# Kernel tuning notes

Hardware: AMD Instinct MI355X
Metric: run time of the kernel (lower is better)

The kernel has to match this reference:

```python
import jax, jax.numpy as jnp
import numpy as np
import math

B, T, N, D = 8, 12, 500, 512  # batch, time(heads), nodes, K*d
FACTOR = 5
SAMPLE_K = min(FACTOR * math.ceil(math.log(N)), N)  # = 35, also n_top (N_Q == N_K)
W_SCALE = 0.02


def setup_inputs() -> dict:
    key = jax.random.key(0)
    ks = jax.random.split(key, 9)
    f32 = jnp.float32
    return {
        "X":   jax.random.normal(ks[0], (B, T, N, D), f32),
        "STE": jax.random.normal(ks[1], (B, T, N, D), f32),
        "Wq":  jax.random.normal(ks[2], (2 * D, D), f32) * W_SCALE,
        "bq":  jnp.zeros((D,), f32),
        "Wk":  jax.random.normal(ks[3], (2 * D, D), f32) * W_SCALE,
        "bk":  jnp.zeros((D,), f32),
        "Wv":  jax.random.normal(ks[4], (2 * D, D), f32) * W_SCALE,
        "bv":  jnp.zeros((D,), f32),
        "sample_idx": jax.random.randint(ks[5], (N, SAMPLE_K), 0, N, jnp.int32),
    }


def reference(X, STE, Wq, bq, Wk, bk, Wv, bv, sample_idx):
    # concat spatial features with spatio-temporal embedding -> projections
    Xc = jnp.concatenate([X, STE], axis=-1)                  # [B,T,N,2D]
    q = jax.nn.relu(Xc @ Wq + bq)                            # [B,T,N,D]
    k = jax.nn.relu(Xc @ Wk + bk)
    v = jax.nn.relu(Xc @ Wv + bv)

    n_top = SAMPLE_K
    # _prob_QK: sampled Q-K scores. Since SAMPLE_K*D >> N, computing the full
    # [B,T,N,N] score matrix and gathering the sampled columns is strictly
    # cheaper in memory than materializing K_sample [B,T,N,S,D] as torch does;
    # the math (Q_K_sample values) is identical.
    scores_full = jnp.einsum('bhld,bhmd->bhlm', q, k)        # [B,T,N,N]
    QK_sample = jnp.take_along_axis(
        scores_full, sample_idx[None, None, :, :], axis=3)   # [B,T,N,S]
    # sparsity measure M = max - mean (mean over L_K = N)
    M = QK_sample.max(axis=-1) - QK_sample.sum(axis=-1) / N  # [B,T,N]
    _, idx = jax.lax.top_k(M, n_top)                         # [B,T,n_top]

    # reduced-query full attention scores (gather rows of full scores == Q_reduce @ K^T)
    scores = jnp.take_along_axis(scores_full, idx[..., None], axis=2)  # [B,T,u,N]
    scores = scores * (1.0 / math.sqrt(D))

    # ProbMask (mask_flag=True): causal mask per selected query position
    j = jnp.arange(N)
    mask = j[None, None, None, :] > idx[..., None]           # [B,T,u,N]
    scores = jnp.where(mask, -jnp.inf, scores)
    attn = jax.nn.softmax(scores, axis=-1)                   # [B,T,u,N]
    ctx_new = jnp.einsum('bhun,bhnd->bhud', attn, v)         # [B,T,u,D]

    # initial context = causal cumsum of V, then scatter-update selected queries
    context = jnp.cumsum(v, axis=2)                          # [B,T,N,D]
    bi = jnp.arange(B)[:, None, None]
    hi = jnp.arange(T)[None, :, None]
    context = context.at[bi, hi, idx].set(ctx_new)
    # .transpose(2,1) in torch -> swap axes 1 and 2
    return context.transpose(0, 2, 1, 3)                     # [B,N,T,D]
```

## Files before the change

### kernel.cpp

```cpp
#include <hip/hip_runtime.h>
#include <math.h>

#define B_    8
#define T_    12
#define BT    96
#define NN    500
#define DD    512
#define KK    1024
#define SK    35
#define MROWS 48000

typedef __bf16 bf16x8 __attribute__((ext_vector_type(8)));
typedef float f32x4 __attribute__((ext_vector_type(4)));
typedef unsigned short u16;
typedef unsigned int u32;
typedef u16 ushort8_t __attribute__((ext_vector_type(8)));
typedef u16 ushort4_t __attribute__((ext_vector_type(4)));

__device__ __forceinline__ u16 bf_hi(float x) {
  __bf16 h = (__bf16)x;
  return __builtin_bit_cast(u16, h);
}
__device__ __forceinline__ float bf_tof(u16 b) {
  unsigned int u = ((unsigned int)b) << 16;
  return __builtin_bit_cast(float, u);
}

__device__ __forceinline__ int lds_off(int row, int kq) {
  return row * 32 + ((kq ^ ((row >> 1) & 3)) * 8);
}

__device__ __forceinline__ void gload_lds16(const u16* g, u16* l) {
  __builtin_amdgcn_global_load_lds(
      (const __attribute__((address_space(1))) u32*)g,
      (__attribute__((address_space(3))) u32*)l, 16, 0, 0);
}

__global__ __launch_bounds__(256) void convW_kernel(
    const float* __restrict__ W, u16* __restrict__ Bth, u16* __restrict__ Btl)
{
  const int n = blockIdx.x;
  const int k0 = threadIdx.x * 4;
  float xs[4];
#pragma unroll
  for (int j = 0; j < 4; ++j) xs[j] = W[(size_t)(k0 + j) * 512 + n];
  ushort4_t hi, lo;
#pragma unroll
  for (int j = 0; j < 4; ++j) {
    u16 h = bf_hi(xs[j]);
    hi[j] = h;
    lo[j] = bf_hi(xs[j] - bf_tof(h));
  }
  *(ushort4_t*)(Bth + (size_t)n * 1024 + k0) = hi;
  *(ushort4_t*)(Btl + (size_t)n * 1024 + k0) = lo;
}

template<int PASSES>
__global__ __launch_bounds__(256) void mfma_proj(
    const float* __restrict__ X, const float* __restrict__ STE,
    const u16* __restrict__ Bth, const u16* __restrict__ Btl,
    const float* __restrict__ bias, float* __restrict__ out)
{
  constexpr int NT = (PASSES == 3) ? 4 : 2;
  __shared__ u16 ldsbuf[2 * NT * 4096];
  const int tid = threadIdx.x;
  const int lane = tid & 63;
  const int wid = tid >> 6;
  const int wm = wid >> 1, wn = wid & 1;
  const int orig = blockIdx.x;
  const int xcd = orig & 7, pos = orig >> 3;
  const int wg = (xcd < 4 ? xcd * 188 : 752 + (xcd - 4) * 187) + pos;
  const int r0 = (wg >> 2) * 128;
  const int c0 = (wg & 3) * 128;
  const int fr = lane & 15, fk = lane >> 4;
  const int rin = lane >> 2;
  const int qq  = lane & 3;

  f32x4 acc[4][4];
#pragma unroll
  for (int m = 0; m < 4; ++m)
#pragma unroll
    for (int n = 0; n < 4; ++n) acc[m][n] = f32x4{0.f, 0.f, 0.f, 0.f};

  auto STAGE = [&](int buf, int kt) {
    u16* bAh = ldsbuf + buf * NT * 4096;
    u16* bBh = bAh + 4096;
    u16* bAl = bAh + 8192;
    u16* bBl = bAh + 12288;
    const int kk0 = kt * 32;
    float4 a0[2], a1[2];
#pragma unroll
    for (int p = 0; p < 2; ++p) {
      const int c = tid + p * 256;
      const int row = c >> 2, kc = c & 3;
      const int col = kk0 + kc * 8;
      const float* src = (col < 512)
          ? (X + (size_t)(r0 + row) * 512 + col)
          : (STE + (size_t)(r0 + row) * 512 + (col - 512));
      a0[p] = *(const float4*)src;
      a1[p] = *(const float4*)(src + 4);
    }
#pragma unroll
    for (int i = 0; i < 2; ++i) {
      const int ch = wid * 2 + i;
      const int row = ch * 16 + rin;
      const int kq = qq ^ ((row >> 1) & 3);
      const size_t gb = (size_t)(c0 + row) * 1024 + kk0 + kq * 8;
      gload_lds16(Bth + gb, bBh + ch * 512);
      if (PASSES == 3) gload_lds16(Btl + gb, bBl + ch * 512);
    }
#pragma unroll
    for (int p = 0; p < 2; ++p) {
      const int c = tid + p * 256;
      const int row = c >> 2, kc = c & 3;
      const int dst = lds_off(row, kc);
      float xs[8] = {a0[p].x, a0[p].y, a0[p].z, a0[p].w,
                     a1[p].x, a1[p].y, a1[p].z, a1[p].w};
      ushort8_t hi, lo;
#pragma unroll
      for (int j = 0; j < 8; ++j) {
        u16 h = bf_hi(xs[j]);
        hi[j] = h;
        if (PASSES == 3) lo[j] = bf_hi(xs[j] - bf_tof(h));
      }
      *(ushort8_t*)&bAh[dst] = hi;
      if (PASSES == 3) *(ushort8_t*)&bAl[dst] = lo;
    }
  };

  STAGE(0, 0);
  __syncthreads();
  int cur = 0;
  for (int kt = 0; kt < 32; ++kt) {
    if (kt + 1 < 32) STAGE(cur ^ 1, kt + 1);
    u16* bAh = ldsbuf + cur * NT * 4096;
    u16* bBh = bAh + 4096;
    u16* bAl = bAh + 8192;
    u16* bBl = bAh + 12288;
    bf16x8 ah[4], al[4];
#pragma unroll
    for (int m = 0; m < 4; ++m) {
      const int off = lds_off(wm * 64 + m * 16 + fr, fk);
      ah[m] = *(const bf16x8*)&bAh[off];
      if (PASSES == 3) al[m] = *(const bf16x8*)&bAl[off];
    }
#pragma unroll
    for (int n = 0; n < 4; ++n) {
      const int off = lds_off(wn * 64 + n * 16 + fr, fk);
      bf16x8 bh = *(const bf16x8*)&bBh[off];
      bf16x8 bl;
      if (PASSES == 3) bl = *(const bf16x8*)&bBl[off];
#pragma unroll
      for (int m = 0; m < 4; ++m) {
        acc[m][n] = __builtin_amdgcn_mfma_f32_16x16x32_bf16(
            ah[m], bh, acc[m][n], 0, 0, 0);
        if (PASSES == 3) {
          acc[m][n] = __builtin_amdgcn_mfma_f32_16x16x32_bf16(
              ah[m], bl, acc[m][n], 0, 0, 0);
          acc[m][n] = __builtin_amdgcn_mfma_f32_16x16x32_bf16(
              al[m], bh, acc[m][n], 0, 0, 0);
        }
      }
    }
    __syncthreads();
    cur ^= 1;
  }

#pragma unroll
  for (int n = 0; n < 4; ++n) {
    const int col = c0 + wn * 64 + n * 16 + fr;
    const float bb = bias[col];
#pragma unroll
    for (int m = 0; m < 4; ++m) {
      const int rowb = r0 + wm * 64 + m * 16 + fk * 4;
#pragma unroll
      for (int r = 0; r < 4; ++r)
        out[(size_t)(rowb + r) * 512 + col] = fmaxf(acc[m][n][r] + bb, 0.f);
    }
  }
}

__global__ __launch_bounds__(256) void sampled_M_kernel(
    const float* __restrict__ q, const float* __restrict__ k,
    const int* __restrict__ sidx, float* __restrict__ Mout)
{
  const int tid = threadIdx.x;
  const int lane = tid & 63, wid = tid >> 6;
  const int bid = blockIdx.x;
  const int xcd = bid & 7, j = bid >> 3;
  const int btg = j / 125, ub = j - btg * 125;
  const int bt = btg * 8 + xcd;
  const int nn = ub * 4 + wid;
  const int n = bt * NN + nn;
  const float* qrow = q + (size_t)n * DD + lane * 8;
  float4 q0 = *(const float4*)qrow;
  float4 q1 = *(const float4*)(qrow + 4);
  const float* kbase = k + (size_t)bt * NN * DD;
  float mx = -INFINITY, sm = 0.f;
  for (int s = 0; s < SK; ++s) {
    int m = sidx[nn * SK + s];
    const float* krow = kbase + (size_t)m * DD + lane * 8;
    float4 k0 = *(const float4*)krow;
    float4 k1 = *(const float4*)(krow + 4);
    float ss = q0.x*k0.x + q0.y*k0.y + q0.z*k0.z + q0.w*k0.w
             + q1.x*k1.x + q1.y*k1.y + q1.z*k1.z + q1.w*k1.w;
#pragma unroll
    for (int off = 32; off > 0; off >>= 1) ss += __shfl_xor(ss, off);
    mx = fmaxf(mx, ss);
    sm += ss;
  }
  if (lane == 0) Mout[n] = mx - sm * (1.0f / (float)NN);
}

__global__ __launch_bounds__(256) void topk_kernel(
    const float* __restrict__ Mb, int* __restrict__ idxb,
    int* __restrict__ sqi, int* __restrict__ su)
{
  const int bt = blockIdx.x;
  const int tid = threadIdx.x;
  __shared__ float mv[NN];
  __shared__ float rv[256];
  __shared__ int ri[256];
  __shared__ int qsel[SK];
  for (int n = tid; n < NN; n += 256) mv[n] = Mb[(size_t)bt * NN + n];
  __syncthreads();
  for (int it = 0; it < SK; ++it) {
    float bv = -INFINITY; int bi = NN;
    for (int n = tid; n < NN; n += 256) {
      float x = mv[n];
      if (x > bv) { bv = x; bi = n; }
    }
    rv[tid] = bv; ri[tid] = bi;
    __syncthreads();
    for (int sft = 128; sft > 0; sft >>= 1) {
      if (tid < sft) {
        float xv = rv[tid + sft]; int xi = ri[tid + sft];
        if (xv > rv[tid] || (xv == rv[tid] && xi < ri[tid])) {
          rv[tid] = xv; ri[tid] = xi;
        }
      }
      __syncthreads();
    }
    if (tid == 0) {
      idxb[bt * SK + it] = ri[0];
      qsel[it] = ri[0];
      mv[ri[0]] = -INFINITY;
    }
    __syncthreads();
  }
  if (tid < SK) {
    int myqi = qsel[tid];
    int rank = 0;
    for (int j = 0; j < SK; ++j) rank += (qsel[j] < myqi);
    sqi[bt * SK + rank] = myqi;
    su[bt * SK + rank] = tid;
  }
}

__global__ __launch_bounds__(256) void attn_part_kernel(
    const float* __restrict__ q, const float* __restrict__ k,
    const float* __restrict__ v, const int* __restrict__ sqi,
    float* __restrict__ pO, float* __restrict__ pm, float* __restrict__ pl)
{
  const int bid = blockIdx.x;
  const int xcd = bid & 7, j = bid >> 3;
  const int btg = j / 35, rem = j - btg * 35;
  const int g = rem / 5, c = rem % 5;
  const int bt = btg * 8 + xcd;
  const int base = bt * SK + g * 5;
  const int c0 = c * 100;
  const int tid = threadIdx.x;
  const int lane = tid & 63, wid = tid >> 6;

  __shared__ float sc[5][100];
  __shared__ int qg[5];
  __shared__ float pmx[5], psm[5];
  if (tid < 5) qg[tid] = sqi[base + tid];
  __syncthreads();
  const int gq = qg[4];
  const int mend = (gq < c0 + 99) ? gq : (c0 + 99);

  float4 qr[5][2];
#pragma unroll
  for (int jj = 0; jj < 5; ++jj) {
    const float* qp = q + ((size_t)bt * NN + qg[jj]) * DD + lane * 8;
    qr[jj][0] = *(const float4*)qp;
    qr[jj][1] = *(const float4*)(qp + 4);
  }
  const float scale = 0.044194173824159216f;

  for (int m = c0 + wid; m <= mend; m += 4) {
    const float* krow = k + ((size_t)bt * NN + m) * DD + lane * 8;
    float4 k0 = *(const float4*)krow;
    float4 k1 = *(const float4*)(krow + 4);
    float p[5];
#pragma unroll
    for (int jj = 0; jj < 5; ++jj) {
      p[jj] = qr[jj][0].x*k0.x + qr[jj][0].y*k0.y
            + qr[jj][0].z*k0.z + qr[jj][0].w*k0.w
            + qr[jj][1].x*k1.x + qr[jj][1].y*k1.y
            + qr[jj][1].z*k1.z + qr[jj][1].w*k1.w;
    }
#pragma unroll
    for (int off = 32; off > 0; off >>= 1)
#pragma unroll
      for (int jj = 0; jj < 5; ++jj) p[jj] += __shfl_xor(p[jj], off);
    if (lane == 0) {
#pragma unroll
      for (int jj = 0; jj < 5; ++jj) sc[jj][m - c0] = p[jj] * scale;
    }
  }
  __syncthreads();

  for (int jj = wid; jj < 5; jj += 4) {
    const int qe = (qg[jj] < c0 + 99) ? qg[jj] : (c0 + 99);
    const int len = qe - c0 + 1;
    float mx = -3e38f;
    for (int i = lane; i < len; i += 64) mx = fmaxf(mx, sc[jj][i]);
#pragma unroll
    for (int off = 32; off > 0; off >>= 1) mx = fmaxf(mx, __shfl_xor(mx, off));
    float sm = 0.f;
    for (int i = lane; i < len; i += 64) {
      float e = __expf(sc[jj][i] - mx);
      sc[jj][i] = e;
      sm += e;
    }
#pragma unroll
    for (int off = 32; off > 0; off >>= 1) sm += __shfl_xor(sm, off);
    if (lane == 0) { pmx[jj] = mx; psm[jj] = sm; }
  }
  __syncthreads();

  float a0[5] = {0.f,0.f,0.f,0.f,0.f}, a1[5] = {0.f,0.f,0.f,0.f,0.f};
  const float* vb = v + (size_t)bt * NN * DD;
  for (int m = c0; m <= mend; ++m) {
    float v0 = vb[(size_t)m * DD + tid];
    float v1 = vb[(size_t)m * DD + tid + 256];
#pragma unroll
    for (int jj = 0; jj < 5; ++jj) {
      if (m <= qg[jj]) {
        float w = sc[jj][m - c0];
        a0[jj] = fmaf(w, v0, a0[jj]);
        a1[jj] = fmaf(w, v1, a1[jj]);
      }
    }
  }

  const int pidx = (bt * 7 + g) * 5 + c;
  if (tid < 5) {
    pm[pidx * 5 + tid] = pmx[tid];
    pl[pidx * 5 + tid] = psm[tid];
  }
#pragma unroll
  for (int jj = 0; jj < 5; ++jj) {
    float* po = pO + ((size_t)(pidx * 5 + jj)) * DD;
    po[tid] = a0[jj];
    po[tid + 256] = a1[jj];
  }
}

__global__ __launch_bounds__(512) void attn_combine_kernel(
    const float* __restrict__ pO, const float* __restrict__ pm,
    const float* __restrict__ pl, const int* __restrict__ su,
    float* __restrict__ ctxn)
{
  const int bid = blockIdx.x;
  const int bt = bid / SK, s = bid % SK;
  const int g = s / 5, jj = s % 5;
  const int d = threadIdx.x;
  __shared__ float w[5];
  __shared__ float linv;
  if (d == 0) {
    float m_[5], l_[5], mx = -3e38f;
#pragma unroll
    for (int c = 0; c < 5; ++c) {
      const int pidx = (bt * 7 + g) * 5 + c;
      m_[c] = pm[pidx * 5 + jj];
      l_[c] = pl[pidx * 5 + jj];
      mx = fmaxf(mx, m_[c]);
    }
    float lt = 0.f;
#pragma unroll
    for (int c = 0; c < 5; ++c) {
      float wc = __expf(m_[c] - mx);
      w[c] = wc;
      lt += wc * l_[c];
    }
    linv = 1.f / lt;
  }
  __syncthreads();
  float o = 0.f;
#pragma unroll
  for (int c = 0; c < 5; ++c) {
    const int pidx = (bt * 7 + g) * 5 + c;
    o = fmaf(w[c], pO[((size_t)(pidx * 5 + jj)) * DD + d], o);
  }
  const int u = su[bt * SK + s];
  ctxn[((size_t)bt * SK + u) * DD + d] = o * linv;
}

__global__ __launch_bounds__(512) void vchunk_sum_kernel(
    const float* __restrict__ v, float* __restrict__ csum)
{
  const int ch = blockIdx.x, bt = blockIdx.y;
  const int d = threadIdx.x;
  const float* vb = v + ((size_t)bt * NN + ch * 50) * DD + d;
  float s = 0.f;
  for (int n = 0; n < 50; ++n) s += vb[(size_t)n * DD];
  csum[((size_t)bt * 10 + ch) * DD + d] = s;
}

__global__ __launch_bounds__(512) void cumsum_scatter2_kernel(
    const float* __restrict__ v, const int* __restrict__ idxb,
    const float* __restrict__ ctxn, const float* __restrict__ csum,
    float* __restrict__ out)
{
  const int ch = blockIdx.x, bt = blockIdx.y;
  const int b = bt / T_, t = bt % T_;
  const int d = threadIdx.x;
  const int n0 = ch * 50;
  __shared__ int sel[50];
  if (threadIdx.x < 50) sel[threadIdx.x] = -1;
  __syncthreads();
  if (threadIdx.x < SK) {
    int qi = idxb[bt * SK + threadIdx.x];
    if (qi >= n0 && qi < n0 + 50) sel[qi - n0] = threadIdx.x;
  }
  __syncthreads();
  float s = 0.f;
  for (int c = 0; c < ch; ++c) s += csum[((size_t)bt * 10 + c) * DD + d];
  for (int i = 0; i < 50; ++i) {
    s += v[((size_t)bt * NN + n0 + i) * DD + d];
    float o = s;
    int u = sel[i];
    if (u >= 0) o = ctxn[((size_t)bt * SK + u) * DD + d];
    out[(((size_t)b * NN + (n0 + i)) * T_ + t) * DD + d] = o;
  }
}

extern "C" void kernel_launch(void* const* d_in, const int* in_sizes, int n_in,
                              void* d_out, int out_size, void* d_ws, size_t ws_size,
                              hipStream_t stream) {
  const float* X   = (const float*)d_in[0];
  const float* STE = (const float*)d_in[1];
  const float* Wq  = (const float*)d_in[2];
  const float* bq  = (const float*)d_in[3];
  const float* Wk  = (const float*)d_in[4];
  const float* bk  = (const float*)d_in[5];
  const float* Wv  = (const float*)d_in[6];
  const float* bv  = (const float*)d_in[7];
  const int* sidx  = (const int*)d_in[8];
  float* out = (float*)d_out;

  float* q    = (float*)d_ws;
  float* k    = q + (size_t)MROWS * DD;
  float* v    = k + (size_t)MROWS * DD;
  float* Mb   = v + (size_t)MROWS * DD;
  int*   idxb = (int*)(Mb + MROWS);
  float* ctxn = (float*)(idxb + BT * SK);
  u16* Bqh = (u16*)(ctxn + (size_t)BT * SK * DD);
  u16* Bql = Bqh + (size_t)512 * 1024;
  u16* Bkh = Bql + (size_t)512 * 1024;
  u16* Bkl = Bkh + (size_t)512 * 1024;
  u16* Bvh = Bkl + (size_t)512 * 1024;
  u16* Bvl = Bvh + (size_t)512 * 1024;
  float* csum = (float*)Bqh;
  int*   sqi  = (int*)Bkh;
  int*   su   = sqi + BT * SK;
  float* pm   = (float*)(su + BT * SK);
  float* pl   = pm + 3360 * 5;
  float* pO   = (float*)d_out;
  (void)ws_size; (void)in_sizes; (void)n_in; (void)out_size;

  convW_kernel<<<512, 256, 0, stream>>>(Wq, Bqh, Bql);
  convW_kernel<<<512, 256, 0, stream>>>(Wk, Bkh, Bkl);
  convW_kernel<<<512, 256, 0, stream>>>(Wv, Bvh, Bvl);

  mfma_proj<3><<<1500, 256, 0, stream>>>(X, STE, Bqh, Bql, bq, q);
  mfma_proj<3><<<1500, 256, 0, stream>>>(X, STE, Bkh, Bkl, bk, k);
  mfma_proj<1><<<1500, 256, 0, stream>>>(X, STE, Bvh, Bvl, bv, v);

  sampled_M_kernel<<<12000, 256, 0, stream>>>(q, k, sidx, Mb);
  topk_kernel<<<BT, 256, 0, stream>>>(Mb, idxb, sqi, su);
  attn_part_kernel<<<3360, 256, 0, stream>>>(q, k, v, sqi, pO, pm, pl);
  attn_combine_kernel<<<3360, 512, 0, stream>>>(pO, pm, pl, su, ctxn);
  dim3 g5(10, BT);
  vchunk_sum_kernel<<<g5, 512, 0, stream>>>(v, csum);
  cumsum_scatter2_kernel<<<g5, 512, 0, stream>>>(v, idxb, ctxn, csum, out);
}
```

Before: 903.1 us.

## Precompute bf16 hi/lo split of input activations and load via async LDS

```diff
diff --git a/kernel.cpp b/kernel.cpp
--- a/kernel.cpp
+++ b/kernel.cpp
@@ -36,6 +36,30 @@
       (__attribute__((address_space(3))) u32*)l, 16, 0, 0);
 }
 
+__global__ __launch_bounds__(256) void convA_kernel(
+    const float* __restrict__ X, const float* __restrict__ STE,
+    u16* __restrict__ Ah, u16* __restrict__ Al)
+{
+  const int r = blockIdx.x * 2 + (threadIdx.x >> 7);
+  const int c0 = (threadIdx.x & 127) * 8;
+  const float* src = (c0 < 512)
+      ? (X + (size_t)r * 512 + c0)
+      : (STE + (size_t)r * 512 + (c0 - 512));
+  float4 x0 = *(const float4*)src;
+  float4 x1 = *(const float4*)(src + 4);
+  float xs[8] = {x0.x, x0.y, x0.z, x0.w, x1.x, x1.y, x1.z, x1.w};
+  ushort8_t hi, lo;
+#pragma unroll
+  for (int j = 0; j < 8; ++j) {
+    u16 h = bf_hi(xs[j]);
+    hi[j] = h;
+    lo[j] = bf_hi(xs[j] - bf_tof(h));
+  }
+  const size_t o = (size_t)r * 1024 + c0;
+  *(ushort8_t*)(Ah + o) = hi;
+  *(ushort8_t*)(Al + o) = lo;
+}
+
 __global__ __launch_bounds__(256) void convW_kernel(
     const float* __restrict__ W, u16* __restrict__ Bth, u16* __restrict__ Btl)
 {
@@ -57,7 +81,7 @@
 
 template<int PASSES>
 __global__ __launch_bounds__(256) void mfma_proj(
-    const float* __restrict__ X, const float* __restrict__ STE,
+    const u16* __restrict__ Ah, const u16* __restrict__ Al,
     const u16* __restrict__ Bth, const u16* __restrict__ Btl,
     const float* __restrict__ bias, float* __restrict__ out)
 {
@@ -88,43 +112,20 @@
     u16* bAl = bAh + 8192;
     u16* bBl = bAh + 12288;
     const int kk0 = kt * 32;
-    float4 a0[2], a1[2];
-#pragma unroll
-    for (int p = 0; p < 2; ++p) {
-      const int c = tid + p * 256;
-      const int row = c >> 2, kc = c & 3;
-      const int col = kk0 + kc * 8;
-      const float* src = (col < 512)
-          ? (X + (size_t)(r0 + row) * 512 + col)
-          : (STE + (size_t)(r0 + row) * 512 + (col - 512));
-      a0[p] = *(const float4*)src;
-      a1[p] = *(const float4*)(src + 4);
-    }
 #pragma unroll
     for (int i = 0; i < 2; ++i) {
       const int ch = wid * 2 + i;
       const int row = ch * 16 + rin;
       const int kq = qq ^ ((row >> 1) & 3);
-      const size_t gb = (size_t)(c0 + row) * 1024 + kk0 + kq * 8;
+      const int off = kk0 + kq * 8;
+      const size_t ga = (size_t)(r0 + row) * 1024 + off;
+      const size_t gb = (size_t)(c0 + row) * 1024 + off;
+      gload_lds16(Ah + ga, bAh + ch * 512);
       gload_lds16(Bth + gb, bBh + ch * 512);
-      if (PASSES == 3) gload_lds16(Btl + gb, bBl + ch * 512);
-    }
-#pragma unroll
-    for (int p = 0; p < 2; ++p) {
-      const int c = tid + p * 256;
-      const int row = c >> 2, kc = c & 3;
-      const int dst = lds_off(row, kc);
-      float xs[8] = {a0[p].x, a0[p].y, a0[p].z, a0[p].w,
-                     a1[p].x, a1[p].y, a1[p].z, a1[p].w};
-      ushort8_t hi, lo;
-#pragma unroll
-      for (int j = 0; j < 8; ++j) {
-        u16 h = bf_hi(xs[j]);
-        hi[j] = h;
-        if (PASSES == 3) lo[j] = bf_hi(xs[j] - bf_tof(h));
+      if (PASSES == 3) {
+        gload_lds16(Al + ga, bAl + ch * 512);
+        gload_lds16(Btl + gb, bBl + ch * 512);
       }
-      *(ushort8_t*)&bAh[dst] = hi;
-      if (PASSES == 3) *(ushort8_t*)&bAl[dst] = lo;
     }
   };
 
@@ -469,16 +470,19 @@
   int*   su   = sqi + BT * SK;
   float* pm   = (float*)(su + BT * SK);
   float* pl   = pm + 3360 * 5;
+  u16* Ah = (u16*)d_out;
+  u16* Al = (u16*)v;
   float* pO   = (float*)d_out;
   (void)ws_size; (void)in_sizes; (void)n_in; (void)out_size;
 
+  convA_kernel<<<MROWS / 2, 256, 0, stream>>>(X, STE, Ah, Al);
   convW_kernel<<<512, 256, 0, stream>>>(Wq, Bqh, Bql);
   convW_kernel<<<512, 256, 0, stream>>>(Wk, Bkh, Bkl);
   convW_kernel<<<512, 256, 0, stream>>>(Wv, Bvh, Bvl);
 
-  mfma_proj<3><<<1500, 256, 0, stream>>>(X, STE, Bqh, Bql, bq, q);
-  mfma_proj<3><<<1500, 256, 0, stream>>>(X, STE, Bkh, Bkl, bk, k);
-  mfma_proj<1><<<1500, 256, 0, stream>>>(X, STE, Bvh, Bvl, bv, v);
+  mfma_proj<3><<<1500, 256, 0, stream>>>(Ah, Al, Bqh, Bql, bq, q);
+  mfma_proj<3><<<1500, 256, 0, stream>>>(Ah, Al, Bkh, Bkl, bk, k);
+  mfma_proj<1><<<1500, 256, 0, stream>>>(Ah, Al, Bvh, Bvl, bv, v);
 
   sampled_M_kernel<<<12000, 256, 0, stream>>>(q, k, sidx, Mb);
   topk_kernel<<<BT, 256, 0, stream>>>(Mb, idxb, sqi, su);
```

New measurement: 925.7 us. +2.5%, slower.
